# Kernel optimization log

Hardware: AMD Instinct MI355X
Metric: run time of the kernel (lower is better)

## Reference

```python
import jax, jax.numpy as jnp
import numpy as np

B, C, H, W = 2, 512, 256, 256
EPS = 1e-5


def setup_inputs() -> dict:
    key = jax.random.key(0)
    ks = jax.random.split(key, 11)
    inp = {
        "x": jax.random.normal(ks[0], (B, C, H, W), dtype=jnp.float32),
        "w1": jax.random.normal(ks[1], (C, 1, H, 1), dtype=jnp.float32) * 0.05,
        "w2": jax.random.normal(ks[2], (C, 1, 1, W), dtype=jnp.float32) * 0.05,
        "g1": jax.random.uniform(ks[3], (C,), dtype=jnp.float32) + 0.5,
        "b1": jax.random.normal(ks[4], (C,), dtype=jnp.float32) * 0.1,
        "g2": jax.random.uniform(ks[5], (C,), dtype=jnp.float32) + 0.5,
        "b2": jax.random.normal(ks[6], (C,), dtype=jnp.float32) * 0.1,
        "lw1": jax.random.normal(ks[7], (2 * C, C), dtype=jnp.float32) * 0.02,
        "lb1": jax.random.normal(ks[8], (2 * C,), dtype=jnp.float32) * 0.02,
        "lw2": jax.random.normal(ks[9], (C, 2 * C), dtype=jnp.float32) * 0.02,
        "lb2": jax.random.normal(ks[10], (C,), dtype=jnp.float32) * 0.02,
    }
    return inp


def _dwconv(x, k):
    # depthwise conv, VALID padding, stride 1; k: [C,1,kh,kw]
    return jax.lax.conv_general_dilated(
        x, k, window_strides=(1, 1), padding="VALID",
        dimension_numbers=("NCHW", "OIHW", "NCHW"),
        feature_group_count=x.shape[1])


def _bn_relu(y, gamma, beta):
    # BatchNorm2d in training mode: biased batch stats over (N,H,W)
    m = jnp.mean(y, axis=(0, 2, 3), keepdims=True)
    v = jnp.var(y, axis=(0, 2, 3), keepdims=True)
    yn = (y - m) * jax.lax.rsqrt(v + EPS)
    return jax.nn.relu(yn * gamma.reshape(1, -1, 1, 1) + beta.reshape(1, -1, 1, 1))


def reference(x, w1, w2, g1, b1, g2, b2, lw1, lb1, lw2, lb2):
    b, c, h, w = x.shape
    xl1 = _bn_relu(_dwconv(x, w1), g1, b1)  # [b,c,1,w]
    xl2 = _bn_relu(_dwconv(x, w2), g2, b2)  # [b,c,h,1]
    # per-(channel,batch) dot product; torch code stacks as [c,b,1] then views (b,c)
    dot_cb = jnp.einsum("bck,bck->cb", xl1[:, :, 0, :], xl2[:, :, :, 0])  # [c,b]
    num = dot_cb.reshape(b, c)  # faithful layout-scrambling view
    num = num @ lw1.T + lb1
    num = num @ lw2.T + lb2
    num = jax.nn.softmax(num, axis=1)  # [b,c]
    return x * num[:, :, None, None]
```

## Files before the change

kernel.cpp:

```cpp
#include <hip/hip_runtime.h>
#include <hip/hip_bf16.h>

#define Bn 2
#define Cn 512
#define Hn 256
#define Wn 256
#define EPSc 1e-5f

typedef float f32x4 __attribute__((ext_vector_type(4)));

__global__ __launch_bounds__(512) void k1_fused(const float* __restrict__ x,
                                                const float* __restrict__ w1,
                                                const float* __restrict__ w2,
                                                const float* __restrict__ g1v,
                                                const float* __restrict__ b1v,
                                                const float* __restrict__ g2v,
                                                const float* __restrict__ b2v,
                                                float* __restrict__ numv) {
    const int c    = blockIdx.x;
    const int tid  = threadIdx.x;
    const int wv   = tid >> 6;
    const int lane = tid & 63;
    const int bb   = wv >> 2;
    const int wq   = wv & 3;

    __shared__ float w1s[Hn];
    __shared__ float s1buf[8][Wn];
    __shared__ float s2s[2][Hn];
    __shared__ float redbuf[8][4];
    __shared__ float stats[4];
    __shared__ float dred[8];

    if (tid < Hn) w1s[tid] = w1[c * Hn + tid];
    __syncthreads();

    const float4 w2v = *(const float4*)(w2 + c * Wn + lane * 4);
    const float* __restrict__ xs = x + (size_t)(bb * Cn + c) * (Hn * Wn);

    float4 acc = make_float4(0.f, 0.f, 0.f, 0.f);
    #pragma unroll 2
    for (int h = wq; h < Hn; h += 4) {
        float4 v = *(const float4*)(xs + h * Wn + lane * 4);
        float wh = w1s[h];
        acc.x += v.x * wh; acc.y += v.y * wh;
        acc.z += v.z * wh; acc.w += v.w * wh;
        float p = v.x * w2v.x + v.y * w2v.y + v.z * w2v.z + v.w * w2v.w;
        #pragma unroll
        for (int off = 32; off; off >>= 1) p += __shfl_xor(p, off, 64);
        if (lane == 0) s2s[bb][h] = p;
    }
    ((float4*)(&s1buf[wv][0]))[lane] = acc;
    __syncthreads();

    const int bI = tid >> 8, k = tid & 255;
    float s1v = s1buf[bI * 4 + 0][k] + s1buf[bI * 4 + 1][k] +
                s1buf[bI * 4 + 2][k] + s1buf[bI * 4 + 3][k];
    float s2v = s2s[bI][k];

    float sum1 = s1v, sq1 = s1v * s1v, sum2 = s2v, sq2 = s2v * s2v;
    #pragma unroll
    for (int off = 32; off; off >>= 1) {
        sum1 += __shfl_xor(sum1, off, 64);
        sq1  += __shfl_xor(sq1,  off, 64);
        sum2 += __shfl_xor(sum2, off, 64);
        sq2  += __shfl_xor(sq2,  off, 64);
    }
    if (lane == 0) {
        redbuf[wv][0] = sum1; redbuf[wv][1] = sq1;
        redbuf[wv][2] = sum2; redbuf[wv][3] = sq2;
    }
    __syncthreads();
    if (tid == 0) {
        float t1 = 0.f, t2 = 0.f, t3 = 0.f, t4 = 0.f;
        #pragma unroll
        for (int q = 0; q < 8; q++) {
            t1 += redbuf[q][0]; t2 += redbuf[q][1];
            t3 += redbuf[q][2]; t4 += redbuf[q][3];
        }
        const float inv = 1.0f / 512.0f;
        float m1 = t1 * inv, m2 = t3 * inv;
        stats[0] = m1;
        stats[1] = rsqrtf(t2 * inv - m1 * m1 + EPSc);
        stats[2] = m2;
        stats[3] = rsqrtf(t4 * inv - m2 * m2 + EPSc);
    }
    __syncthreads();

    const float m1 = stats[0], r1 = stats[1], m2 = stats[2], r2 = stats[3];
    const float G1 = g1v[c], B1 = b1v[c], G2 = g2v[c], B2 = b2v[c];

    float a = fmaxf((s1v - m1) * r1 * G1 + B1, 0.f);
    float e = fmaxf((s2v - m2) * r2 * G2 + B2, 0.f);
    float p = a * e;
    #pragma unroll
    for (int off = 32; off; off >>= 1) p += __shfl_xor(p, off, 64);
    if (lane == 0) dred[wv] = p;
    __syncthreads();
    if (tid < 2)
        numv[c * 2 + tid] = dred[tid * 4 + 0] + dred[tid * 4 + 1] +
                            dred[tid * 4 + 2] + dred[tid * 4 + 3];
}

__global__ __launch_bounds__(256) void k3_fc1(const float* __restrict__ numv,
                                              const float* __restrict__ lw1,
                                              const float* __restrict__ lb1,
                                              float* __restrict__ h1) {
    const int wid  = blockIdx.x * 4 + (threadIdx.x >> 6);
    const int lane = threadIdx.x & 63;
    const int bb = wid >> 10, j = wid & 1023;
    const float* __restrict__ row = lw1 + (size_t)j * Cn;
    const float* __restrict__ nv  = numv + bb * Cn;
    float p = 0.f;
    #pragma unroll
    for (int m = 0; m < 2; m++) {
        float4 a = *(const float4*)(row + lane * 4 + m * 256);
        float4 n = *(const float4*)(nv  + lane * 4 + m * 256);
        p += a.x * n.x + a.y * n.y + a.z * n.z + a.w * n.w;
    }
    #pragma unroll
    for (int off = 32; off; off >>= 1) p += __shfl_xor(p, off, 64);
    if (lane == 0) h1[bb * 1024 + j] = p + lb1[j];
}

__global__ __launch_bounds__(256) void k4_fc2(const float* __restrict__ h1,
                                              const float* __restrict__ lw2,
                                              const float* __restrict__ lb2,
                                              float* __restrict__ h2) {
    const int wid  = blockIdx.x * 4 + (threadIdx.x >> 6);
    const int lane = threadIdx.x & 63;
    const int bb = wid >> 9, c = wid & 511;
    const float* __restrict__ row = lw2 + (size_t)c * 1024;
    const float* __restrict__ hv  = h1 + bb * 1024;
    float p = 0.f;
    #pragma unroll
    for (int m = 0; m < 4; m++) {
        float4 a = *(const float4*)(row + lane * 4 + m * 256);
        float4 n = *(const float4*)(hv  + lane * 4 + m * 256);
        p += a.x * n.x + a.y * n.y + a.z * n.z + a.w * n.w;
    }
    #pragma unroll
    for (int off = 32; off; off >>= 1) p += __shfl_xor(p, off, 64);
    if (lane == 0) h2[bb * Cn + c] = p + lb2[c];
}

__global__ __launch_bounds__(256) void k6_softmax_scale(const float* __restrict__ x,
                                                        const float* __restrict__ h2,
                                                        float* __restrict__ out, int n4) {
    __shared__ float h2s[1024];
    __shared__ float scls[1024];
    __shared__ float mxs[2], sms[2];
    const int t = threadIdx.x;

    #pragma unroll
    for (int j = 0; j < 4; j++) h2s[t + 256 * j] = h2[t + 256 * j];
    __syncthreads();

    const int wv = t >> 6, lane = t & 63;
    if (wv < 2) {
        float mx = -3.402823466e+38f;
        #pragma unroll
        for (int j = 0; j < 8; j++) mx = fmaxf(mx, h2s[wv * 512 + lane + 64 * j]);
        #pragma unroll
        for (int off = 32; off; off >>= 1) mx = fmaxf(mx, __shfl_xor(mx, off, 64));
        float sm = 0.f;
        #pragma unroll
        for (int j = 0; j < 8; j++) sm += expf(h2s[wv * 512 + lane + 64 * j] - mx);
        #pragma unroll
        for (int off = 32; off; off >>= 1) sm += __shfl_xor(sm, off, 64);
        if (lane == 0) { mxs[wv] = mx; sms[wv] = sm; }
    }
    __syncthreads();
    #pragma unroll
    for (int j = 0; j < 4; j++) {
        int idx = t + 256 * j;
        int r = idx >> 9;
        scls[idx] = expf(h2s[idx] - mxs[r]) / sms[r];
    }
    __syncthreads();

    int i = blockIdx.x * 256 + t;
    const int stride = gridDim.x * 256;
    for (; i < n4; i += stride) {
        f32x4 v = ((const f32x4*)x)[i];
        float s = scls[i >> 14];
        f32x4 r = v * s;
        __builtin_nontemporal_store(r, ((f32x4*)out) + i);
    }
}

extern "C" void kernel_launch(void* const* d_in, const int* in_sizes, int n_in,
                              void* d_out, int out_size, void* d_ws, size_t ws_size,
                              hipStream_t stream) {
    const float* x   = (const float*)d_in[0];
    const float* w1  = (const float*)d_in[1];
    const float* w2  = (const float*)d_in[2];
    const float* g1  = (const float*)d_in[3];
    const float* b1  = (const float*)d_in[4];
    const float* g2  = (const float*)d_in[5];
    const float* b2  = (const float*)d_in[6];
    const float* lw1 = (const float*)d_in[7];
    const float* lb1 = (const float*)d_in[8];
    const float* lw2 = (const float*)d_in[9];
    const float* lb2 = (const float*)d_in[10];
    float* out = (float*)d_out;

    float* ws   = (float*)d_ws;
    float* numv = ws;
    float* h1   = ws + 1024;
    float* h2   = ws + 3072;

    k1_fused<<<Cn, 512, 0, stream>>>(x, w1, w2, g1, b1, g2, b2, numv);
    k3_fc1<<<512, 256, 0, stream>>>(numv, lw1, lb1, h1);
    k4_fc2<<<256, 256, 0, stream>>>(h1, lw2, lb2, h2);

    const int n4 = (Bn * Cn * Hn * Wn) / 4;
    k6_softmax_scale<<<4096, 256, 0, stream>>>(x, h2, out, n4);
}
```

Measured before the change: 508.9 us.

## Fuse FC1, FC2 and softmax into one kernel with a grid-wide atomic barrier

Replaces the separate fc1 and fc2 launches with a single 128-block kernel that uses an atomic-counter spin barrier between the two matrix-vector stages. Block 0 then computes the softmax once and writes the per-channel scales to the workspace, so the 4096 blocks of the scale kernel no longer each recompute the softmax. This removes one launch, and the redundant per-block exp and reduction work from the memory-bound final pass. The spin barrier relies on all 128 blocks being resident at the same time, and the counter is reset inside k1.

```diff
diff --git a/kernel.cpp b/kernel.cpp
--- a/kernel.cpp
+++ b/kernel.cpp
@@ -6,6 +6,7 @@
 #define Hn 256
 #define Wn 256
 #define EPSc 1e-5f
+#define K345_BLOCKS 128
 
 typedef float f32x4 __attribute__((ext_vector_type(4)));
 
@@ -16,13 +17,16 @@
                                                 const float* __restrict__ b1v,
                                                 const float* __restrict__ g2v,
                                                 const float* __restrict__ b2v,
-                                                float* __restrict__ numv) {
+                                                float* __restrict__ numv,
+                                                int* __restrict__ cnt) {
     const int c    = blockIdx.x;
     const int tid  = threadIdx.x;
     const int wv   = tid >> 6;
     const int lane = tid & 63;
     const int bb   = wv >> 2;
     const int wq   = wv & 3;
+
+    if (c == 0 && tid < 2) cnt[tid] = 0;
 
     __shared__ float w1s[Hn];
     __shared__ float s1buf[8][Wn];
@@ -101,70 +105,96 @@
                             dred[tid * 4 + 2] + dred[tid * 4 + 3];
 }
 
-__global__ __launch_bounds__(256) void k3_fc1(const float* __restrict__ numv,
-                                              const float* __restrict__ lw1,
-                                              const float* __restrict__ lb1,
-                                              float* __restrict__ h1) {
-    const int wid  = blockIdx.x * 4 + (threadIdx.x >> 6);
-    const int lane = threadIdx.x & 63;
-    const int bb = wid >> 10, j = wid & 1023;
-    const float* __restrict__ row = lw1 + (size_t)j * Cn;
-    const float* __restrict__ nv  = numv + bb * Cn;
-    float p = 0.f;
-    #pragma unroll
-    for (int m = 0; m < 2; m++) {
-        float4 a = *(const float4*)(row + lane * 4 + m * 256);
-        float4 n = *(const float4*)(nv  + lane * 4 + m * 256);
-        p += a.x * n.x + a.y * n.y + a.z * n.z + a.w * n.w;
-    }
-    #pragma unroll
-    for (int off = 32; off; off >>= 1) p += __shfl_xor(p, off, 64);
-    if (lane == 0) h1[bb * 1024 + j] = p + lb1[j];
-}
-
-__global__ __launch_bounds__(256) void k4_fc2(const float* __restrict__ h1,
-                                              const float* __restrict__ lw2,
-                                              const float* __restrict__ lb2,
-                                              float* __restrict__ h2) {
-    const int wid  = blockIdx.x * 4 + (threadIdx.x >> 6);
-    const int lane = threadIdx.x & 63;
-    const int bb = wid >> 9, c = wid & 511;
-    const float* __restrict__ row = lw2 + (size_t)c * 1024;
-    const float* __restrict__ hv  = h1 + bb * 1024;
-    float p = 0.f;
-    #pragma unroll
-    for (int m = 0; m < 4; m++) {
-        float4 a = *(const float4*)(row + lane * 4 + m * 256);
-        float4 n = *(const float4*)(hv  + lane * 4 + m * 256);
-        p += a.x * n.x + a.y * n.y + a.z * n.z + a.w * n.w;
-    }
-    #pragma unroll
-    for (int off = 32; off; off >>= 1) p += __shfl_xor(p, off, 64);
-    if (lane == 0) h2[bb * Cn + c] = p + lb2[c];
-}
-
-__global__ __launch_bounds__(256) void k6_softmax_scale(const float* __restrict__ x,
-                                                        const float* __restrict__ h2,
-                                                        float* __restrict__ out, int n4) {
-    __shared__ float h2s[1024];
-    __shared__ float scls[1024];
+__global__ __launch_bounds__(256) void k345_fc(const float* __restrict__ numv,
+                                               const float* __restrict__ lw1,
+                                               const float* __restrict__ lb1,
+                                               const float* __restrict__ lw2,
+                                               const float* __restrict__ lb2,
+                                               float* __restrict__ h1,
+                                               float* __restrict__ h2,
+                                               float* __restrict__ scl,
+                                               int* __restrict__ cnt) {
+    __shared__ float nv_s[1024];
+    __shared__ float h1_s[2048];
     __shared__ float mxs[2], sms[2];
-    const int t = threadIdx.x;
-
-    #pragma unroll
-    for (int j = 0; j < 4; j++) h2s[t + 256 * j] = h2[t + 256 * j];
-    __syncthreads();
-
-    const int wv = t >> 6, lane = t & 63;
+    const int tid  = threadIdx.x;
+    const int wv   = tid >> 6;
+    const int lane = tid & 63;
+
+    #pragma unroll
+    for (int j = 0; j < 4; j++) nv_s[tid + 256 * j] = numv[tid + 256 * j];
+    __syncthreads();
+
+    #pragma unroll
+    for (int q = 0; q < 4; q++) {
+        const int out = blockIdx.x * 16 + wv * 4 + q;
+        const int bb = out >> 10, j = out & 1023;
+        const float* __restrict__ row = lw1 + (size_t)j * Cn;
+        float p = 0.f;
+        #pragma unroll
+        for (int m = 0; m < 2; m++) {
+            float4 a = *(const float4*)(row + lane * 4 + m * 256);
+            float4 n = *(const float4*)(&nv_s[bb * 512 + lane * 4 + m * 256]);
+            p += a.x * n.x + a.y * n.y + a.z * n.z + a.w * n.w;
+        }
+        #pragma unroll
+        for (int off = 32; off; off >>= 1) p += __shfl_xor(p, off, 64);
+        if (lane == 0) h1[bb * 1024 + j] = p + lb1[j];
+    }
+
+    __threadfence();
+    __syncthreads();
+    if (tid == 0) {
+        atomicAdd(&cnt[0], 1);
+        while (atomicAdd(&cnt[0], 0) < K345_BLOCKS) { }
+    }
+    __syncthreads();
+    __threadfence();
+
+    #pragma unroll
+    for (int j = 0; j < 8; j++) h1_s[tid + 256 * j] = h1[tid + 256 * j];
+    __syncthreads();
+
+    #pragma unroll
+    for (int q = 0; q < 2; q++) {
+        const int out = blockIdx.x * 8 + wv * 2 + q;
+        const int bb = out >> 9, c = out & 511;
+        const float* __restrict__ row = lw2 + (size_t)c * 1024;
+        float p = 0.f;
+        #pragma unroll
+        for (int m = 0; m < 4; m++) {
+            float4 a = *(const float4*)(row + lane * 4 + m * 256);
+            float4 n = *(const float4*)(&h1_s[bb * 1024 + lane * 4 + m * 256]);
+            p += a.x * n.x + a.y * n.y + a.z * n.z + a.w * n.w;
+        }
+        #pragma unroll
+        for (int off = 32; off; off >>= 1) p += __shfl_xor(p, off, 64);
+        if (lane == 0) h2[bb * Cn + c] = p + lb2[c];
+    }
+
+    __threadfence();
+    __syncthreads();
+    if (tid == 0) atomicAdd(&cnt[1], 1);
+    if (blockIdx.x != 0) return;
+    if (tid == 0) {
+        while (atomicAdd(&cnt[1], 0) < K345_BLOCKS) { }
+    }
+    __syncthreads();
+    __threadfence();
+
+    #pragma unroll
+    for (int j = 0; j < 4; j++) nv_s[tid + 256 * j] = h2[tid + 256 * j];
+    __syncthreads();
+
     if (wv < 2) {
         float mx = -3.402823466e+38f;
         #pragma unroll
-        for (int j = 0; j < 8; j++) mx = fmaxf(mx, h2s[wv * 512 + lane + 64 * j]);
+        for (int j = 0; j < 8; j++) mx = fmaxf(mx, nv_s[wv * 512 + lane + 64 * j]);
         #pragma unroll
         for (int off = 32; off; off >>= 1) mx = fmaxf(mx, __shfl_xor(mx, off, 64));
         float sm = 0.f;
         #pragma unroll
-        for (int j = 0; j < 8; j++) sm += expf(h2s[wv * 512 + lane + 64 * j] - mx);
+        for (int j = 0; j < 8; j++) sm += expf(nv_s[wv * 512 + lane + 64 * j] - mx);
         #pragma unroll
         for (int off = 32; off; off >>= 1) sm += __shfl_xor(sm, off, 64);
         if (lane == 0) { mxs[wv] = mx; sms[wv] = sm; }
@@ -172,10 +202,19 @@
     __syncthreads();
     #pragma unroll
     for (int j = 0; j < 4; j++) {
-        int idx = t + 256 * j;
+        int idx = tid + 256 * j;
         int r = idx >> 9;
-        scls[idx] = expf(h2s[idx] - mxs[r]) / sms[r];
-    }
+        scl[idx] = expf(nv_s[idx] - mxs[r]) / sms[r];
+    }
+}
+
+__global__ __launch_bounds__(256) void k6_scale(const float* __restrict__ x,
+                                                const float* __restrict__ scl,
+                                                float* __restrict__ out, int n4) {
+    __shared__ float scls[1024];
+    const int t = threadIdx.x;
+    #pragma unroll
+    for (int j = 0; j < 4; j++) scls[t + 256 * j] = scl[t + 256 * j];
     __syncthreads();
 
     int i = blockIdx.x * 256 + t;
@@ -208,11 +247,12 @@
     float* numv = ws;
     float* h1   = ws + 1024;
     float* h2   = ws + 3072;
-
-    k1_fused<<<Cn, 512, 0, stream>>>(x, w1, w2, g1, b1, g2, b2, numv);
-    k3_fc1<<<512, 256, 0, stream>>>(numv, lw1, lb1, h1);
-    k4_fc2<<<256, 256, 0, stream>>>(h1, lw2, lb2, h2);
+    float* scl  = ws + 4096;
+    int*   cnt  = (int*)(ws + 5120);
+
+    k1_fused<<<Cn, 512, 0, stream>>>(x, w1, w2, g1, b1, g2, b2, numv, cnt);
+    k345_fc<<<K345_BLOCKS, 256, 0, stream>>>(numv, lw1, lb1, lw2, lb2, h1, h2, scl, cnt);
 
     const int n4 = (Bn * Cn * Hn * Wn) / 4;
-    k6_softmax_scale<<<4096, 256, 0, stream>>>(x, h2, out, n4);
-}
+    k6_scale<<<4096, 256, 0, stream>>>(x, scl, out, n4);
+}
```

Result: slower. 535.4 us (+5.2%).
